# Kernel tuning notes

Hardware: AMD Instinct MI355X
Metric: run time of the kernel (lower is better)

The kernel has to match this reference:

```python
import jax, jax.numpy as jnp
import numpy as np

B, T, D = 8, 4096, 1024
H, HD = 8, 128            # head_dim = ceil(D/H)
P = H * HD                # proj_dim = 1024
OUT = 1024
WIN, STRIDE = 64, 32


def _window_index(seq_len, win, stride):
    # mirrors the Python start-list construction in RollingAttentionPooling.forward
    starts = list(range(0, max(1, seq_len), stride))
    if starts and starts[-1] + win < seq_len:
        starts.append(seq_len - win)
    starts = sorted(set(max(0, s) for s in starts))
    idx = np.asarray(starts)[:, None] + np.arange(win)[None, :]
    valid = idx < seq_len
    idx = np.minimum(idx, seq_len - 1)
    return jnp.asarray(idx, dtype=jnp.int32), jnp.asarray(valid)


def setup_inputs() -> dict:
    key = jax.random.key(0)
    k0, k1, k2, k3 = jax.random.split(key, 4)
    x = jax.random.normal(k0, (B, T, D), dtype=jnp.float32)
    w_kv = jax.random.normal(k1, (D, 2 * P), dtype=jnp.float32) * 0.02
    query = jax.random.normal(k2, (H, HD), dtype=jnp.float32)
    w_out_w = jax.random.normal(k3, (OUT, P), dtype=jnp.float32) * 0.02
    w_out_b = jnp.zeros((OUT,), dtype=jnp.float32)
    return {"x": x, "w_kv": w_kv, "query": query, "w_out_w": w_out_w, "w_out_b": w_out_b}


def reference(x, w_kv, query, w_out_w, w_out_b):
    bsz, seq_len, _ = x.shape
    # K/V projection computed once for the whole sequence (same math as
    # recomputing per-window, since windows are slices of x).
    kv = (x @ w_kv).reshape(bsz, seq_len, 2, H, HD)
    k = kv[:, :, 0]                                   # (B, T, H, HD)
    v = kv[:, :, 1]                                   # (B, T, H, HD)
    logits = jnp.einsum('bthd,hd->bht', k, query) / jnp.sqrt(jnp.float32(HD))

    idx, valid = _window_index(seq_len, WIN, STRIDE)
    lw = logits[:, :, idx]
    lw = jnp.where(valid[None, None], lw, -jnp.inf)
    scores = jax.nn.softmax(lw.astype(jnp.float32), axis=-1).astype(v.dtype)
    vw = v[:, idx]
    pooled = jnp.einsum('bhwt,bwthd->bwhd', scores, vw)
    pooled = pooled.reshape(bsz, idx.shape[0], P)     # (B, W, P)
    out_w = pooled @ w_out_w.T + w_out_b              # (B, W, OUT)
    return out_w.mean(axis=1)                         # (B, OUT)
```

## Files before the change

kernel.cpp:

```cpp
#include <hip/hip_runtime.h>

#define B_ 8
#define T_ 4096
#define D_ 1024
#define H_ 8
#define HD_ 128
#define P_ 1024
#define OUT_ 1024
#define W_ 128
#define NC_ 64
#define CHUNK_ 64
#define NPC_ 64
#define PCH_ 16

__global__ void __launch_bounds__(256) k_qproj(const float* __restrict__ w_kv,
                                               const float* __restrict__ query,
                                               float* __restrict__ qp) {
  int d = blockIdx.x;
  int t = threadIdx.x;
  float4 wv = ((const float4*)(w_kv + (size_t)d * (2 * P_)))[t];
  float4 qv = ((const float4*)query)[t];
  float a = wv.x * qv.x + wv.y * qv.y + wv.z * qv.z + wv.w * qv.w;
#pragma unroll
  for (int off = 16; off; off >>= 1) a += __shfl_xor(a, off, 64);
  if ((t & 31) == 0) {
    int h = t >> 5;
    qp[h * D_ + d] = a * 0.08838834764831845f;
  }
}

__global__ void __launch_bounds__(256) k_logits(const float* __restrict__ x,
                                                const float* __restrict__ qp,
                                                float* __restrict__ logits) {
  __shared__ float s_qp[H_ * D_];
  for (int i = threadIdx.x; i < H_ * D_ / 4; i += 256)
    ((float4*)s_qp)[i] = ((const float4*)qp)[i];
  __syncthreads();
  int wid = threadIdx.x >> 6, lane = threadIdx.x & 63;
  int nw = gridDim.x * 4;
  for (int pr = blockIdx.x * 4 + wid; pr < B_ * T_ / 2; pr += nw) {
    int row0 = pr * 2;
    const float4* xr0 = (const float4*)(x + (size_t)row0 * D_);
    const float4* xr1 = (const float4*)(x + (size_t)(row0 + 1) * D_);
    float4 xv0[4], xv1[4];
#pragma unroll
    for (int j = 0; j < 4; ++j) { xv0[j] = xr0[lane + 64 * j]; xv1[j] = xr1[lane + 64 * j]; }
    float acc0[H_], acc1[H_];
#pragma unroll
    for (int h = 0; h < H_; ++h) {
      const float4* qh = (const float4*)(s_qp + h * D_);
      float a0 = 0.f, a1 = 0.f;
#pragma unroll
      for (int j = 0; j < 4; ++j) {
        float4 q = qh[lane + 64 * j];
        a0 += xv0[j].x * q.x + xv0[j].y * q.y + xv0[j].z * q.z + xv0[j].w * q.w;
        a1 += xv1[j].x * q.x + xv1[j].y * q.y + xv1[j].z * q.z + xv1[j].w * q.w;
      }
      acc0[h] = a0; acc1[h] = a1;
    }
#pragma unroll
    for (int h = 0; h < H_; ++h) {
      float a0 = acc0[h], a1 = acc1[h];
#pragma unroll
      for (int off = 32; off; off >>= 1) {
        a0 += __shfl_down(a0, off, 64);
        a1 += __shfl_down(a1, off, 64);
      }
      if (lane == 0) {
        int b = row0 >> 12, t = row0 & (T_ - 1);
        logits[((b * H_ + h) << 12) + t] = a0;
        logits[((b * H_ + h) << 12) + t + 1] = a1;
      }
    }
  }
}

__global__ void __launch_bounds__(128) k_weights(const float* __restrict__ logits,
                                                 float* __restrict__ weight) {
  int bh = blockIdx.x;
  const float* L = logits + (size_t)bh * T_;
  __shared__ float sl[T_];
  __shared__ float sm[W_], srs[W_];
  for (int i = threadIdx.x; i < T_ / 4; i += 128)
    ((float4*)sl)[i] = ((const float4*)L)[i];
  __syncthreads();
  {
    int w = threadIdx.x;
    int start = w * 32;
    int cnt = min(64, T_ - start);
    float m = -1e30f;
    for (int i = 0; i < cnt; ++i) m = fmaxf(m, sl[start + i]);
    float s = 0.f;
    for (int i = 0; i < cnt; ++i) s += __expf(sl[start + i] - m);
    sm[w] = m;
    srs[w] = 1.0f / s;
  }
  __syncthreads();
  const float invW = 1.0f / (float)W_;
  for (int t = threadIdx.x; t < T_; t += 128) {
    float l = sl[t];
    int w1 = t >> 5;
    float acc = __expf(l - sm[w1]) * srs[w1];
    if (w1 > 0) acc += __expf(l - sm[w1 - 1]) * srs[w1 - 1];
    weight[(size_t)bh * T_ + t] = acc * invW;
  }
}

__global__ void __launch_bounds__(256) k_yacc(const float* __restrict__ x,
                                              const float* __restrict__ weight,
                                              float* __restrict__ partial) {
  int b = blockIdx.x >> 6;
  int c = blockIdx.x & 63;
  int t0 = c * CHUNK_;
  __shared__ float sw[H_][CHUNK_];
  for (int i = threadIdx.x; i < H_ * CHUNK_; i += 256) {
    int h = i / CHUNK_, tt = i % CHUNK_;
    sw[h][tt] = weight[((b * H_ + h) << 12) + t0 + tt];
  }
  __syncthreads();
  float4 acc[H_];
#pragma unroll
  for (int h = 0; h < H_; ++h) acc[h] = make_float4(0.f, 0.f, 0.f, 0.f);
  const float4* xb = (const float4*)(x + ((size_t)b * T_ + t0) * D_);
  for (int tt = 0; tt < CHUNK_; ++tt) {
    float4 xv = xb[tt * (D_ / 4) + threadIdx.x];
#pragma unroll
    for (int h = 0; h < H_; ++h) {
      float wv = sw[h][tt];
      acc[h].x += wv * xv.x; acc[h].y += wv * xv.y;
      acc[h].z += wv * xv.z; acc[h].w += wv * xv.w;
    }
  }
  float4* pp = (float4*)(partial + (((size_t)(c * B_ + b) * H_) << 10));
#pragma unroll
  for (int h = 0; h < H_; ++h) pp[h * (D_ / 4) + threadIdx.x] = acc[h];
}

__global__ void __launch_bounds__(256) k_reduce_y(const float* __restrict__ partial,
                                                  float* __restrict__ y) {
  int i = blockIdx.x * blockDim.x + threadIdx.x;
  float4 a = make_float4(0.f, 0.f, 0.f, 0.f);
  const float4* p = (const float4*)partial;
#pragma unroll 8
  for (int c = 0; c < NC_; ++c) {
    float4 v = p[(size_t)c * (B_ * H_ * D_ / 4) + i];
    a.x += v.x; a.y += v.y; a.z += v.z; a.w += v.w;
  }
  ((float4*)y)[i] = a;
}

__global__ void __launch_bounds__(256) k_pooled_part(const float* __restrict__ y,
                                                     const float* __restrict__ w_kv,
                                                     float* __restrict__ ppart) {
  int c = blockIdx.x;
  int d0 = c * PCH_;
  int t = threadIdx.x;
  int h = t >> 5;
  __shared__ float sy[PCH_][B_ * H_];
  for (int i = t; i < PCH_ * B_ * H_; i += 256) {
    int dd = i >> 6, bh = i & 63;
    sy[dd][bh] = y[((size_t)bh << 10) + d0 + dd];
  }
  __syncthreads();
  float4 acc[B_];
#pragma unroll
  for (int b = 0; b < B_; ++b) acc[b] = make_float4(0.f, 0.f, 0.f, 0.f);
#pragma unroll
  for (int dd = 0; dd < PCH_; ++dd) {
    float4 wv = ((const float4*)(w_kv + (size_t)(d0 + dd) * (2 * P_) + P_))[t];
#pragma unroll
    for (int b = 0; b < B_; ++b) {
      float yv = sy[dd][b * H_ + h];
      acc[b].x += yv * wv.x; acc[b].y += yv * wv.y;
      acc[b].z += yv * wv.z; acc[b].w += yv * wv.w;
    }
  }
#pragma unroll
  for (int b = 0; b < B_; ++b)
    ((float4*)(ppart + (((size_t)c * B_ + b) << 10)))[t] = acc[b];
}

__global__ void __launch_bounds__(256) k_reduce_pooled(const float* __restrict__ ppart,
                                                       float* __restrict__ pooled) {
  int i = blockIdx.x * 256 + threadIdx.x;
  int b = i >> 8, p4 = i & 255;
  float4 a = make_float4(0.f, 0.f, 0.f, 0.f);
  const float4* p = (const float4*)ppart;
#pragma unroll 8
  for (int c = 0; c < NPC_; ++c) {
    float4 v = p[((c * B_ + b) << 8) + p4];
    a.x += v.x; a.y += v.y; a.z += v.z; a.w += v.w;
  }
  ((float4*)pooled)[i] = a;
}

__global__ void __launch_bounds__(256) k_out(const float* __restrict__ pooled,
                                             const float* __restrict__ w_out_w,
                                             const float* __restrict__ w_out_b,
                                             float* __restrict__ out) {
  int wid = threadIdx.x >> 6, lane = threadIdx.x & 63;
  int o = blockIdx.x * 4 + wid;
  const float4* wr = (const float4*)(w_out_w + (size_t)o * P_);
  float4 wv[4];
#pragma unroll
  for (int j = 0; j < 4; ++j) wv[j] = wr[lane + 64 * j];
  float res[B_];
#pragma unroll
  for (int b = 0; b < B_; ++b) {
    const float4* pb = (const float4*)(pooled + b * P_);
    float a = 0.f;
#pragma unroll
    for (int j = 0; j < 4; ++j) {
      float4 pv = pb[lane + 64 * j];
      a += wv[j].x * pv.x + wv[j].y * pv.y + wv[j].z * pv.z + wv[j].w * pv.w;
    }
#pragma unroll
    for (int off = 32; off; off >>= 1) a += __shfl_down(a, off, 64);
    res[b] = a;
  }
  if (lane == 0) {
    float bias = w_out_b[o];
#pragma unroll
    for (int b = 0; b < B_; ++b) out[b * OUT_ + o] = res[b] + bias;
  }
}

extern "C" void kernel_launch(void* const* d_in, const int* in_sizes, int n_in,
                              void* d_out, int out_size, void* d_ws, size_t ws_size,
                              hipStream_t stream) {
  const float* x       = (const float*)d_in[0];
  const float* w_kv    = (const float*)d_in[1];
  const float* query   = (const float*)d_in[2];
  const float* w_out_w = (const float*)d_in[3];
  const float* w_out_b = (const float*)d_in[4];
  float* out = (float*)d_out;

  float* ws = (float*)d_ws;
  float* qp      = ws;
  float* logits  = qp + H_ * D_;
  float* weight  = logits + B_ * H_ * T_;
  float* partial = weight + B_ * H_ * T_;
  float* y       = partial + (size_t)NC_ * B_ * H_ * D_;
  float* pooled  = y + B_ * H_ * D_;
  float* ppart   = partial;

  k_qproj<<<D_, 256, 0, stream>>>(w_kv, query, qp);
  k_logits<<<2048, 256, 0, stream>>>(x, qp, logits);
  k_weights<<<B_ * H_, 128, 0, stream>>>(logits, weight);
  k_yacc<<<B_ * NC_, 256, 0, stream>>>(x, weight, partial);
  k_reduce_y<<<(B_ * H_ * D_ / 4) / 256, 256, 0, stream>>>(partial, y);
  k_pooled_part<<<NPC_, 256, 0, stream>>>(y, w_kv, ppart);
  k_reduce_pooled<<<(B_ * P_ / 4) / 256, 256, 0, stream>>>(ppart, pooled);
  k_out<<<OUT_ / 4, 256, 0, stream>>>(pooled, w_out_w, w_out_b, out);
}
```

Baseline: 288.6 us.

## Use transpose-style butterfly reduction for logits and finer k_yacc chunking

```diff
diff --git a/kernel.cpp b/kernel.cpp
--- a/kernel.cpp
+++ b/kernel.cpp
@@ -8,8 +8,6 @@
 #define P_ 1024
 #define OUT_ 1024
 #define W_ 128
-#define NC_ 64
-#define CHUNK_ 64
 #define NPC_ 64
 #define PCH_ 16
 
@@ -40,12 +38,12 @@
   int nw = gridDim.x * 4;
   for (int pr = blockIdx.x * 4 + wid; pr < B_ * T_ / 2; pr += nw) {
     int row0 = pr * 2;
-    const float4* xr0 = (const float4*)(x + (size_t)row0 * D_);
-    const float4* xr1 = (const float4*)(x + (size_t)(row0 + 1) * D_);
+    const float4* xr0 = (const float4*)(x + ((size_t)row0 << 10));
+    const float4* xr1 = (const float4*)(x + ((size_t)(row0 + 1) << 10));
     float4 xv0[4], xv1[4];
 #pragma unroll
     for (int j = 0; j < 4; ++j) { xv0[j] = xr0[lane + 64 * j]; xv1[j] = xr1[lane + 64 * j]; }
-    float acc0[H_], acc1[H_];
+    float p[16];
 #pragma unroll
     for (int h = 0; h < H_; ++h) {
       const float4* qh = (const float4*)(s_qp + h * D_);
@@ -56,21 +54,29 @@
         a0 += xv0[j].x * q.x + xv0[j].y * q.y + xv0[j].z * q.z + xv0[j].w * q.w;
         a1 += xv1[j].x * q.x + xv1[j].y * q.y + xv1[j].z * q.z + xv1[j].w * q.w;
       }
-      acc0[h] = a0; acc1[h] = a1;
-    }
-#pragma unroll
-    for (int h = 0; h < H_; ++h) {
-      float a0 = acc0[h], a1 = acc1[h];
-#pragma unroll
-      for (int off = 32; off; off >>= 1) {
-        a0 += __shfl_down(a0, off, 64);
-        a1 += __shfl_down(a1, off, 64);
+      p[h] = a0; p[8 + h] = a1;
+    }
+#pragma unroll
+    for (int s = 0; s < 4; ++s) {
+      const int m = 1 << s;
+      const int HN = 8 >> s;
+      bool hi = (lane & m) != 0;
+#pragma unroll
+      for (int i = 0; i < HN; ++i) {
+        float keep = hi ? p[HN + i] : p[i];
+        float sent = hi ? p[i] : p[HN + i];
+        float recv = __shfl_xor(sent, m, 64);
+        p[i] = keep + recv;
       }
-      if (lane == 0) {
-        int b = row0 >> 12, t = row0 & (T_ - 1);
-        logits[((b * H_ + h) << 12) + t] = a0;
-        logits[((b * H_ + h) << 12) + t + 1] = a1;
-      }
+    }
+    float v = p[0];
+    v += __shfl_xor(v, 16, 64);
+    v += __shfl_xor(v, 32, 64);
+    if (lane < 16) {
+      int r = lane & 1;
+      int h = ((lane & 2) ? 4 : 0) + ((lane & 4) ? 2 : 0) + ((lane & 8) ? 1 : 0);
+      int b = row0 >> 12, t = row0 & (T_ - 1);
+      logits[((b * H_ + h) << 12) + t + r] = v;
     }
   }
 }
@@ -108,13 +114,14 @@
 
 __global__ void __launch_bounds__(256) k_yacc(const float* __restrict__ x,
                                               const float* __restrict__ weight,
-                                              float* __restrict__ partial) {
-  int b = blockIdx.x >> 6;
-  int c = blockIdx.x & 63;
-  int t0 = c * CHUNK_;
-  __shared__ float sw[H_][CHUNK_];
-  for (int i = threadIdx.x; i < H_ * CHUNK_; i += 256) {
-    int h = i / CHUNK_, tt = i % CHUNK_;
+                                              float* __restrict__ partial,
+                                              int chunk) {
+  int c = blockIdx.x;
+  int b = blockIdx.y;
+  int t0 = c * chunk;
+  __shared__ float sw[H_][64];
+  for (int i = threadIdx.x; i < H_ * chunk; i += 256) {
+    int h = i / chunk, tt = i - h * chunk;
     sw[h][tt] = weight[((b * H_ + h) << 12) + t0 + tt];
   }
   __syncthreads();
@@ -122,7 +129,8 @@
 #pragma unroll
   for (int h = 0; h < H_; ++h) acc[h] = make_float4(0.f, 0.f, 0.f, 0.f);
   const float4* xb = (const float4*)(x + ((size_t)b * T_ + t0) * D_);
-  for (int tt = 0; tt < CHUNK_; ++tt) {
+#pragma unroll 4
+  for (int tt = 0; tt < chunk; ++tt) {
     float4 xv = xb[tt * (D_ / 4) + threadIdx.x];
 #pragma unroll
     for (int h = 0; h < H_; ++h) {
@@ -137,12 +145,12 @@
 }
 
 __global__ void __launch_bounds__(256) k_reduce_y(const float* __restrict__ partial,
-                                                  float* __restrict__ y) {
+                                                  float* __restrict__ y, int nc) {
   int i = blockIdx.x * blockDim.x + threadIdx.x;
   float4 a = make_float4(0.f, 0.f, 0.f, 0.f);
   const float4* p = (const float4*)partial;
 #pragma unroll 8
-  for (int c = 0; c < NC_; ++c) {
+  for (int c = 0; c < nc; ++c) {
     float4 v = p[(size_t)c * (B_ * H_ * D_ / 4) + i];
     a.x += v.x; a.y += v.y; a.z += v.z; a.w += v.w;
   }
@@ -235,20 +243,24 @@
   const float* w_out_b = (const float*)d_in[4];
   float* out = (float*)d_out;
 
+  size_t need128 = ((size_t)8192 + 262144 + 262144 + (size_t)128 * B_ * H_ * D_ + 65536 + 8192) * 4;
+  int nc = (ws_size >= need128) ? 128 : 64;
+  int chunk = T_ / nc;
+
   float* ws = (float*)d_ws;
   float* qp      = ws;
   float* logits  = qp + H_ * D_;
   float* weight  = logits + B_ * H_ * T_;
   float* partial = weight + B_ * H_ * T_;
-  float* y       = partial + (size_t)NC_ * B_ * H_ * D_;
+  float* y       = partial + (size_t)nc * B_ * H_ * D_;
   float* pooled  = y + B_ * H_ * D_;
   float* ppart   = partial;
 
   k_qproj<<<D_, 256, 0, stream>>>(w_kv, query, qp);
-  k_logits<<<2048, 256, 0, stream>>>(x, qp, logits);
+  k_logits<<<1280, 256, 0, stream>>>(x, qp, logits);
   k_weights<<<B_ * H_, 128, 0, stream>>>(logits, weight);
-  k_yacc<<<B_ * NC_, 256, 0, stream>>>(x, weight, partial);
-  k_reduce_y<<<(B_ * H_ * D_ / 4) / 256, 256, 0, stream>>>(partial, y);
+  k_yacc<<<dim3(nc, B_), 256, 0, stream>>>(x, weight, partial, chunk);
+  k_reduce_y<<<(B_ * H_ * D_ / 4) / 256, 256, 0, stream>>>(partial, y, nc);
   k_pooled_part<<<NPC_, 256, 0, stream>>>(y, w_kv, ppart);
   k_reduce_pooled<<<(B_ * P_ / 4) / 256, 256, 0, stream>>>(ppart, pooled);
   k_out<<<OUT_ / 4, 256, 0, stream>>>(pooled, w_out_w, w_out_b, out);
```

Result: slower. 329.2 us (+14.1%).
